# Optimization experiments

Hardware: AMD Instinct MI355X
Metric: run time of the kernel (lower is better)

The kernel has to match this reference:

```python
import jax, jax.numpy as jnp
import numpy as np

B, L, DIM = 1, 2048, 512
DHEAD = 64
HEADS = DIM // DHEAD  # 8
KS = 127              # kernel_size (odd)
EXP = 4


def setup_inputs() -> dict:
    key = jax.random.key(0)
    ks = jax.random.split(key, 8)
    sc = 0.02
    rnd = lambda k, shape: (jax.random.normal(k, shape, jnp.float32) * sc)
    return {
        "x": jax.random.normal(ks[0], (B, L, DIM), jnp.float32),
        "ln1_g": jnp.ones((DIM,), jnp.float32),
        "ln1_b": jnp.zeros((DIM,), jnp.float32),
        "qkv_w": rnd(ks[1], (DIM, 3 * DIM)),
        "qkv_b": jnp.zeros((3 * DIM,), jnp.float32),
        "rpb": rnd(ks[2], (HEADS, 2 * KS - 1)),
        "proj_w": rnd(ks[3], (DIM, DIM)),
        "proj_b": jnp.zeros((DIM,), jnp.float32),
        "ln2_g": jnp.ones((DIM,), jnp.float32),
        "ln2_b": jnp.zeros((DIM,), jnp.float32),
        "ff1_w": rnd(ks[4], (DIM, DIM * EXP)),
        "ff1_b": jnp.zeros((DIM * EXP,), jnp.float32),
        "ff2_w": rnd(ks[5], (DIM * EXP, DIM)),
        "ff2_b": jnp.zeros((DIM,), jnp.float32),
    }


def _layernorm(x, g, b, eps=1e-5):
    m = x.mean(-1, keepdims=True)
    v = ((x - m) ** 2).mean(-1, keepdims=True)
    return (x - m) * jax.lax.rsqrt(v + eps) * g + b


def _neighborhood_attn_1d(x, qkv_w, qkv_b, rpb, proj_w, proj_b):
    # NATTEN NeighborhoodAttention1D: window of KS keys per query, clamped
    # at sequence edges so every query sees exactly KS keys (requires L >= KS).
    b, l, dim = x.shape
    qkv = (x @ qkv_w + qkv_b).reshape(b, l, 3, HEADS, DHEAD)
    q, k, v = qkv[:, :, 0], qkv[:, :, 1], qkv[:, :, 2]  # [b,l,h,d]
    scale = DHEAD ** -0.5
    # window start per query, clamped to stay in-bounds
    starts = jnp.clip(jnp.arange(l) - KS // 2, 0, l - KS)          # [l]
    idx = starts[:, None] + jnp.arange(KS)                         # [l,KS]
    kg = k[:, idx]                                                 # [b,l,KS,h,d]
    vg = v[:, idx]                                                 # [b,l,KS,h,d]
    logits = jnp.einsum('blhd,blkhd->blhk', q * scale, kg)         # [b,l,h,KS]
    # relative-position bias: index = (j - i) + (KS - 1), in [0, 2KS-2]
    bias_idx = idx - jnp.arange(l)[:, None] + (KS - 1)             # [l,KS]
    logits = logits + rpb[:, bias_idx].transpose(1, 0, 2)[None]    # [1,l,h,KS]
    attn = jax.nn.softmax(logits, axis=-1)
    out = jnp.einsum('blhk,blkhd->blhd', attn, vg).reshape(b, l, dim)
    return out @ proj_w + proj_b


def reference(x, ln1_g, ln1_b, qkv_w, qkv_b, rpb, proj_w, proj_b,
              ln2_g, ln2_b, ff1_w, ff1_b, ff2_w, ff2_b):
    x = x + _neighborhood_attn_1d(_layernorm(x, ln1_g, ln1_b),
                                  qkv_w, qkv_b, rpb, proj_w, proj_b)
    h = _layernorm(x, ln2_g, ln2_b)
    h = jax.nn.gelu(h @ ff1_w + ff1_b, approximate=False) @ ff2_w + ff2_b
    return x + h
```

## Files before the change

kernel.cpp:

```cpp
#include <hip/hip_runtime.h>
#include <hip/hip_bf16.h>

static constexpr int Lc     = 2048;
static constexpr int DIMc   = 512;
static constexpr int HEADSc = 8;
static constexpr int DHEADc = 64;
static constexpr int KSc    = 127;
static constexpr int NQKVc  = 1536;

typedef __attribute__((ext_vector_type(8))) short short8;
typedef __attribute__((ext_vector_type(4))) float f32x4;
typedef unsigned short u16;
typedef unsigned int u32;

__device__ __forceinline__ float b2f(u16 s) {
  return __uint_as_float(((u32)s) << 16);
}
__device__ __forceinline__ u16 f2b(float x) {
  u32 u = __float_as_uint(x);
  return (u16)((u + 0x7fffu + ((u >> 16) & 1u)) >> 16);
}
__device__ __forceinline__ void gload16(const void* g, void* l) {
  __builtin_amdgcn_global_load_lds(
      (const __attribute__((address_space(1))) u32*)g,
      (__attribute__((address_space(3))) u32*)l, 16, 0, 0);
}

__global__ __launch_bounds__(256) void prep_kernel(
    const float* __restrict__ w0, const float* __restrict__ w1,
    const float* __restrict__ w2, const float* __restrict__ w3,
    u16* __restrict__ o0, u16* __restrict__ o1, u16* __restrict__ o2,
    u16* __restrict__ o3, const float* __restrict__ xin,
    const float* __restrict__ g, const float* __restrict__ b,
    u16* __restrict__ lnout) {
  __shared__ float tl[32][33];
  __shared__ float rs[4], rq[4], stat[2];
  const int tid = threadIdx.x;
  if (blockIdx.x >= 3072) {
    const int row = blockIdx.x - 3072;
    const float* rp = xin + (size_t)row * DIMc;
    float v0 = rp[tid];
    float v1 = rp[tid + 256];
    float s = v0 + v1;
    float sq = v0 * v0 + v1 * v1;
#pragma unroll
    for (int o = 32; o > 0; o >>= 1) {
      s += __shfl_down(s, o);
      sq += __shfl_down(sq, o);
    }
    const int wid = tid >> 6, lane = tid & 63;
    if (lane == 0) { rs[wid] = s; rq[wid] = sq; }
    __syncthreads();
    if (tid == 0) {
      float S = rs[0] + rs[1] + rs[2] + rs[3];
      float Q = rq[0] + rq[1] + rq[2] + rq[3];
      float m = S / DIMc;
      float var = Q / DIMc - m * m;
      stat[0] = m;
      stat[1] = rsqrtf(var + 1e-5f);
    }
    __syncthreads();
    const float m = stat[0], r = stat[1];
    lnout[(size_t)row * DIMc + tid] = f2b((v0 - m) * r * g[tid] + b[tid]);
    lnout[(size_t)row * DIMc + tid + 256] =
        f2b((v1 - m) * r * g[tid + 256] + b[tid + 256]);
    return;
  }
  int t = blockIdx.x;
  const float* W;
  u16* O;
  int K, N;
  if (t < 768)       { W = w0; O = o0; K = 512;  N = 1536; }
  else if (t < 1024) { W = w1; O = o1; K = 512;  N = 512;  t -= 768; }
  else if (t < 2048) { W = w2; O = o2; K = 512;  N = 2048; t -= 1024; }
  else               { W = w3; O = o3; K = 2048; N = 512;  t -= 2048; }
  const int nt = N >> 5;
  const int by = t / nt, bx = t % nt;
  const int c = tid & 31, r0 = tid >> 5;
#pragma unroll
  for (int i = 0; i < 4; ++i) {
    const int r = r0 + i * 8;
    tl[r][c] = W[(size_t)(by * 32 + r) * N + bx * 32 + c];
  }
  __syncthreads();
#pragma unroll
  for (int i = 0; i < 4; ++i) {
    const int r = r0 + i * 8;
    O[(size_t)(bx * 32 + r) * K + by * 32 + c] = f2b(tl[c][r]);
  }
}

__global__ __launch_bounds__(256) void ln2_kernel(const float* __restrict__ in,
                                                  const float* __restrict__ g,
                                                  const float* __restrict__ b,
                                                  u16* __restrict__ out) {
  const int row = blockIdx.x;
  const int tid = threadIdx.x;
  const float* rp = in + (size_t)row * DIMc;
  float v0 = rp[tid];
  float v1 = rp[tid + 256];
  float s = v0 + v1;
  float sq = v0 * v0 + v1 * v1;
  __shared__ float rs[4], rq[4], stat[2];
#pragma unroll
  for (int o = 32; o > 0; o >>= 1) {
    s += __shfl_down(s, o);
    sq += __shfl_down(sq, o);
  }
  const int wid = tid >> 6, lane = tid & 63;
  if (lane == 0) { rs[wid] = s; rq[wid] = sq; }
  __syncthreads();
  if (tid == 0) {
    float S = rs[0] + rs[1] + rs[2] + rs[3];
    float Q = rq[0] + rq[1] + rq[2] + rq[3];
    float m = S / DIMc;
    float var = Q / DIMc - m * m;
    stat[0] = m;
    stat[1] = rsqrtf(var + 1e-5f);
  }
  __syncthreads();
  const float m = stat[0], r = stat[1];
  out[(size_t)row * DIMc + tid] = f2b((v0 - m) * r * g[tid] + b[tid]);
  out[(size_t)row * DIMc + tid + 256] =
      f2b((v1 - m) * r * g[tid + 256] + b[tid + 256]);
}

template <int OP, typename OUT_T>
__global__ __launch_bounds__(128) void mfma_gemm(
    const u16* __restrict__ A, const u16* __restrict__ Bt,
    const float* __restrict__ bias, const float* __restrict__ res,
    OUT_T* __restrict__ C, int M, int N, int K) {
  constexpr int BK = 64;
  __shared__ __align__(16) u16 As[2][64 * BK];
  __shared__ __align__(16) u16 Bs[2][64 * BK];
  const int tid = threadIdx.x;
  const int wave = tid >> 6, lane = tid & 63;
  const int m0 = blockIdx.y * 64, n0 = blockIdx.x * 64;
  const int wn = wave * 32;
  const int T = K / BK;

  f32x4 acc[4][2] = {};

  const int fr = lane & 15;
  const int hi = lane >> 4;

  const int lrow = wave * 8 + (lane >> 3);
  const int lcol = ((lane & 7) ^ (lane >> 3)) * 8;

#define STAGE(k0, buf)                                                        \
  {                                                                           \
    _Pragma("unroll") for (int p = 0; p < 4; ++p) {                           \
      gload16(A + (size_t)(m0 + p * 16 + lrow) * K + (k0) + lcol,             \
              &As[buf][p * 1024 + wave * 512]);                               \
      gload16(Bt + (size_t)(n0 + p * 16 + lrow) * K + (k0) + lcol,            \
              &Bs[buf][p * 1024 + wave * 512]);                               \
    }                                                                         \
  }

  STAGE(0, 0);
  STAGE(BK, 1);

  for (int t = 0; t < T; ++t) {
    const int cur = t & 1;
    if (t + 1 < T) {
      asm volatile("s_waitcnt vmcnt(8)" ::: "memory");
    } else {
      asm volatile("s_waitcnt vmcnt(0)" ::: "memory");
    }
    __builtin_amdgcn_s_barrier();

    short8 af[4][2], bf[2][2];
#pragma unroll
    for (int i = 0; i < 4; ++i) {
      const int row = i * 16 + fr;
      const char* rb = (const char*)As[cur] + row * 128;
#pragma unroll
      for (int ks = 0; ks < 2; ++ks)
        af[i][ks] =
            *(const short8*)(rb + ((ks * 64 + hi * 16) ^ ((fr & 7) << 4)));
    }
#pragma unroll
    for (int j = 0; j < 2; ++j) {
      const int row = wn + j * 16 + fr;
      const char* rb = (const char*)Bs[cur] + row * 128;
#pragma unroll
      for (int ks = 0; ks < 2; ++ks)
        bf[j][ks] =
            *(const short8*)(rb + ((ks * 64 + hi * 16) ^ ((fr & 7) << 4)));
    }
    asm volatile("s_waitcnt lgkmcnt(0)" ::: "memory");
    __builtin_amdgcn_sched_barrier(0);
    __builtin_amdgcn_s_barrier();

    if (t + 2 < T) STAGE((t + 2) * BK, cur);

#pragma unroll
    for (int ks = 0; ks < 2; ++ks)
#pragma unroll
      for (int i = 0; i < 4; ++i)
#pragma unroll
        for (int j = 0; j < 2; ++j)
          acc[i][j] = __builtin_amdgcn_mfma_f32_16x16x32_bf16(
              af[i][ks], bf[j][ks], acc[i][j], 0, 0, 0);
  }
#undef STAGE

  const int cl = lane & 15;
  const int rbase = (lane >> 4) * 4;
#pragma unroll
  for (int i = 0; i < 4; ++i) {
#pragma unroll
    for (int j = 0; j < 2; ++j) {
      const int c = n0 + wn + j * 16 + cl;
      const float bv = bias[c];
#pragma unroll
      for (int r = 0; r < 4; ++r) {
        const int row = m0 + i * 16 + rbase + r;
        float v = acc[i][j][r] + bv;
        if (OP == 1) v = 0.5f * v * (1.0f + erff(v * 0.70710678118f));
        ((u16*)C)[(size_t)row * N + c] = f2b(v);
      }
    }
  }
}

__global__ __launch_bounds__(256, 1) void mfma_gemm_ks(
    const u16* __restrict__ A, const u16* __restrict__ Bt,
    const float* __restrict__ bias, const float* __restrict__ res,
    float* __restrict__ C, int M, int N, int K) {
  constexpr int BK = 32;
  __shared__ __align__(16) char LB[65536];
  const int tid = threadIdx.x;
  const int wave = tid >> 6, lane = tid & 63;
  const int m0 = blockIdx.y * 64, n0 = blockIdx.x * 64;
  const int kslice = K >> 2;
  const int kbeg = wave * kslice;
  const int T = kslice / BK;
  char* myb = LB + wave * 16384;

  f32x4 acc[4][4] = {};
  const int fr = lane & 15;
  const int hi = lane >> 4;

  const int lrow = lane >> 2;
  const int lcol = ((lane & 3) ^ ((lane >> 2) & 3)) * 8;

#define KSTAGE(k0, b)                                                         \
  {                                                                           \
    _Pragma("unroll") for (int p = 0; p < 4; ++p) {                           \
      gload16(A + (size_t)(m0 + p * 16 + lrow) * K + (k0) + lcol,             \
              myb + (b) * 8192 + p * 1024);                                   \
      gload16(Bt + (size_t)(n0 + p * 16 + lrow) * K + (k0) + lcol,            \
              myb + (b) * 8192 + 4096 + p * 1024);                            \
    }                                                                         \
  }

  KSTAGE(kbeg, 0);
  KSTAGE(kbeg + BK, 1);

  for (int t = 0; t < T; ++t) {
    const int cur = t & 1;
    if (t + 1 < T) {
      asm volatile("s_waitcnt vmcnt(8)" ::: "memory");
    } else {
      asm volatile("s_waitcnt vmcnt(0)" ::: "memory");
    }

    short8 af[4], bf[4];
#pragma unroll
    for (int i = 0; i < 4; ++i) {
      const char* rb = myb + cur * 8192 + (i * 16 + fr) * 64;
      af[i] = *(const short8*)(rb + ((hi * 16) ^ ((fr & 3) << 4)));
    }
#pragma unroll
    for (int j = 0; j < 4; ++j) {
      const char* rb = myb + cur * 8192 + 4096 + (j * 16 + fr) * 64;
      bf[j] = *(const short8*)(rb + ((hi * 16) ^ ((fr & 3) << 4)));
    }
    asm volatile("s_waitcnt lgkmcnt(0)" ::: "memory");
    __builtin_amdgcn_sched_barrier(0);

    if (t + 2 < T) KSTAGE(kbeg + (t + 2) * BK, cur);

    __builtin_amdgcn_s_setprio(1);
#pragma unroll
    for (int i = 0; i < 4; ++i)
#pragma unroll
      for (int j = 0; j < 4; ++j)
        acc[i][j] = __builtin_amdgcn_mfma_f32_16x16x32_bf16(af[i], bf[j],
                                                            acc[i][j], 0, 0, 0);
    __builtin_amdgcn_s_setprio(0);
  }
#undef KSTAGE

  __syncthreads();
  float* red = (float*)LB;
  const int rbase = hi * 4;
#pragma unroll
  for (int i = 0; i < 4; ++i)
#pragma unroll
    for (int j = 0; j < 4; ++j)
#pragma unroll
      for (int r = 0; r < 4; ++r)
        red[wave * 4096 + (i * 16 + rbase + r) * 64 + j * 16 + fr] =
            acc[i][j][r];
  __syncthreads();
#pragma unroll
  for (int q = 0; q < 4; ++q) {
    const int idx = q * 1024 + tid * 4;
    const int row = idx >> 6, col = idx & 63;
    f32x4 s = *(const f32x4*)&red[idx];
#pragma unroll
    for (int w = 1; w < 4; ++w) s += *(const f32x4*)&red[w * 4096 + idx];
    const f32x4 bb = *(const f32x4*)&bias[n0 + col];
    const size_t o = (size_t)(m0 + row) * N + n0 + col;
    const f32x4 rr = *(const f32x4*)&res[o];
    s += bb + rr;
    *(f32x4*)&C[o] = s;
  }
}

__global__ __launch_bounds__(256) void attn_mfma(const u16* __restrict__ qkv,
                                                 const float* __restrict__ rpb,
                                                 u16* __restrict__ out) {
  constexpr int NR = 192, NT = 12, PP = 200;
  __shared__ __align__(16) u16 Ks[NR * DHEADc];
  __shared__ __align__(16) u16 Vt[DHEADc * NR];
  __shared__ __align__(16) u16 Ps[4][16 * PP];
  __shared__ float rp[2 * KSc - 1];
  const int h = blockIdx.y, l0 = blockIdx.x * 64, tid = threadIdx.x;
  const int wv = tid >> 6, lane = tid & 63;
  const int fr = lane & 15, hi = lane >> 4;

  int s_min = l0 - 63;
  if (s_min < 0) s_min = 0;
  if (s_min > Lc - KSc) s_min = Lc - KSc;

  for (int i = tid; i < 2 * KSc - 1; i += 256) rp[i] = rpb[h * (2 * KSc - 1) + i];

#pragma unroll
  for (int rd = 0; rd < 6; ++rd) {
    const int linear = rd * 4096 + wv * 1024 + lane * 16;
    const int row = linear >> 7;
    const int seg = (linear >> 4) & 7;
    const int segp = seg ^ (row & 7);
    int gl = s_min + row;
    if (gl > Lc - 1) gl = Lc - 1;
    gload16(qkv + (size_t)gl * NQKVc + DIMc + h * DHEADc + segp * 8,
            (char*)Ks + rd * 4096 + wv * 1024);
  }

#pragma unroll
  for (int rd = 0; rd < 3; ++rd) {
    const int t = rd * 256 + tid;
    const int rpair = t >> 3, seg = t & 7;
    const int r0 = rpair * 2;
    int g0 = s_min + r0, g1 = s_min + r0 + 1;
    if (g0 > Lc - 1) g0 = Lc - 1;
    if (g1 > Lc - 1) g1 = Lc - 1;
    const short8 a =
        *(const short8*)(qkv + (size_t)g0 * NQKVc + 2 * DIMc + h * DHEADc + seg * 8);
    const short8 bq =
        *(const short8*)(qkv + (size_t)g1 * NQKVc + 2 * DIMc + h * DHEADc + seg * 8);
#pragma unroll
    for (int j = 0; j < 8; ++j) {
      const int d = seg * 8 + j;
      int byte = d * (NR * 2) + r0 * 2;
      byte ^= (d & 7) << 4;
      *(u32*)((char*)Vt + byte) =
          ((u32)(u16)a[j]) | (((u32)(u16)bq[j]) << 16);
    }
  }

  const int lq = l0 + wv * 16 + fr;
  short8 qf[2];
#pragma unroll
  for (int ks = 0; ks < 2; ++ks)
    qf[ks] = *(const short8*)(qkv + (size_t)lq * NQKVc + h * DHEADc + ks * 32 + hi * 8);

  __syncthreads();

  f32x4 S[NT] = {};
  __builtin_amdgcn_s_setprio(1);
#pragma unroll
  for (int jt = 0; jt < NT; ++jt) {
#pragma unroll
    for (int ks = 0; ks < 2; ++ks) {
      int byte = (jt * 16 + fr) * 128 + ks * 64 + hi * 16;
      byte ^= (fr & 7) << 4;
      const short8 kf = *(const short8*)((const char*)Ks + byte);
      S[jt] = __builtin_amdgcn_mfma_f32_16x16x32_bf16(qf[ks], kf, S[jt], 0, 0, 0);
    }
  }
  __builtin_amdgcn_s_setprio(0);

  float inv4[4];
#pragma unroll
  for (int r = 0; r < 4; ++r) {
    const int l = l0 + wv * 16 + hi * 4 + r;
    int st = l - 63;
    if (st < 0) st = 0;
    if (st > Lc - KSc) st = Lc - KSc;
    float mx = -3e38f;
#pragma unroll
    for (int jt = 0; jt < NT; ++jt) {
      const int pos = s_min + jt * 16 + fr;
      const int j = pos - st;
      float v = -3e38f;
      if (j >= 0 && j <= KSc - 1) v = S[jt][r] * 0.125f + rp[pos - l + KSc - 1];
      S[jt][r] = v;
      mx = fmaxf(mx, v);
    }
#pragma unroll
    for (int o = 1; o < 16; o <<= 1) mx = fmaxf(mx, __shfl_xor(mx, o));
    float sum = 0.f;
#pragma unroll
    for (int jt = 0; jt < NT; ++jt) {
      const float e = __expf(S[jt][r] - mx);
      S[jt][r] = e;
      sum += e;
    }
#pragma unroll
    for (int o = 1; o < 16; o <<= 1) sum += __shfl_xor(sum, o);
    inv4[r] = 1.f / sum;
  }

#pragma unroll
  for (int jt = 0; jt < NT; ++jt)
#pragma unroll
    for (int r = 0; r < 4; ++r)
      Ps[wv][(hi * 4 + r) * PP + jt * 16 + fr] = f2b(S[jt][r] * inv4[r]);

  f32x4 O[4] = {};
  __builtin_amdgcn_s_setprio(1);
#pragma unroll
  for (int ks = 0; ks < 6; ++ks) {
    const short8 pa =
        *(const short8*)((const char*)Ps[wv] + fr * (PP * 2) + ks * 64 + hi * 16);
#pragma unroll
    for (int dt = 0; dt < 4; ++dt) {
      int byte = (dt * 16 + fr) * (NR * 2) + ks * 64 + hi * 16;
      byte ^= (fr & 7) << 4;
      const short8 vb = *(const short8*)((const char*)Vt + byte);
      O[dt] = __builtin_amdgcn_mfma_f32_16x16x32_bf16(pa, vb, O[dt], 0, 0, 0);
    }
  }
  __builtin_amdgcn_s_setprio(0);

#pragma unroll
  for (int dt = 0; dt < 4; ++dt)
#pragma unroll
    for (int r = 0; r < 4; ++r)
      out[(size_t)(l0 + wv * 16 + hi * 4 + r) * DIMc + h * DHEADc + dt * 16 + fr] =
          f2b(O[dt][r]);
}

extern "C" void kernel_launch(void* const* d_in, const int* in_sizes, int n_in,
                              void* d_out, int out_size, void* d_ws,
                              size_t ws_size, hipStream_t stream) {
  const float* x      = (const float*)d_in[0];
  const float* ln1_g  = (const float*)d_in[1];
  const float* ln1_b  = (const float*)d_in[2];
  const float* qkv_w  = (const float*)d_in[3];
  const float* qkv_b  = (const float*)d_in[4];
  const float* rpb    = (const float*)d_in[5];
  const float* proj_w = (const float*)d_in[6];
  const float* proj_b = (const float*)d_in[7];
  const float* ln2_g  = (const float*)d_in[8];
  const float* ln2_b  = (const float*)d_in[9];
  const float* ff1_w  = (const float*)d_in[10];
  const float* ff1_b  = (const float*)d_in[11];
  const float* ff2_w  = (const float*)d_in[12];
  const float* ff2_b  = (const float*)d_in[13];
  float* out = (float*)d_out;

  char* ws = (char*)d_ws;
  u16*   lnbuf   = (u16*)(ws);
  u16*   qkvbuf  = (u16*)(ws + ((size_t)2  << 20));
  u16*   attnbuf = (u16*)(ws + ((size_t)8  << 20));
  float* x2      = (float*)(ws + ((size_t)10 << 20));
  u16*   ff1buf  = (u16*)(ws + ((size_t)14 << 20));
  u16*   wt_qkv  = (u16*)(ws + ((size_t)22 << 20));
  u16*   wt_proj = (u16*)(ws + ((size_t)23 << 20) + ((size_t)512 << 10));
  u16*   wt_ff1  = (u16*)(ws + ((size_t)24 << 20));
  u16*   wt_ff2  = (u16*)(ws + ((size_t)26 << 20));

  prep_kernel<<<5120, 256, 0, stream>>>(qkv_w, proj_w, ff1_w, ff2_w, wt_qkv,
                                        wt_proj, wt_ff1, wt_ff2, x, ln1_g,
                                        ln1_b, lnbuf);
  mfma_gemm<0, u16><<<dim3(NQKVc / 64, Lc / 64), 128, 0, stream>>>(
      lnbuf, wt_qkv, qkv_b, nullptr, qkvbuf, Lc, NQKVc, DIMc);
  attn_mfma<<<dim3(Lc / 64, HEADSc), 256, 0, stream>>>(qkvbuf, rpb, attnbuf);
  mfma_gemm_ks<<<dim3(DIMc / 64, Lc / 64), 256, 0, stream>>>(
      attnbuf, wt_proj, proj_b, x, x2, Lc, DIMc, DIMc);
  ln2_kernel<<<Lc, 256, 0, stream>>>(x2, ln2_g, ln2_b, lnbuf);
  mfma_gemm<1, u16><<<dim3(4 * DIMc / 64, Lc / 64), 128, 0, stream>>>(
      lnbuf, wt_ff1, ff1_b, nullptr, ff1buf, Lc, 4 * DIMc, DIMc);
  mfma_gemm_ks<<<dim3(DIMc / 64, Lc / 64), 256, 0, stream>>>(
      ff1buf, wt_ff2, ff2_b, x2, out, Lc, DIMc, 4 * DIMc);
}
```

Baseline: 67.05 us.

## Fold non-QKV weight transposes into the QKV GEMM launch and vectorize transposes

The prep kernel now transposes and converts only the QKV weight and runs LayerNorm1. The proj, ff1 and ff2 weight transposes move into extra blocks of a new fused QKV GEMM kernel, so that memory-bound conversion work runs alongside the compute-bound GEMM tiles instead of delaying it. The transpose tiles also switch to float4 loads and packed ushort4 stores. In exchange, the GEMM kernel carries extra LDS for the transpose tile and a branch, which may reduce occupancy for the GEMM blocks.

```diff
diff --git a/kernel.cpp b/kernel.cpp
--- a/kernel.cpp
+++ b/kernel.cpp
@@ -27,17 +27,14 @@
 }
 
 __global__ __launch_bounds__(256) void prep_kernel(
-    const float* __restrict__ w0, const float* __restrict__ w1,
-    const float* __restrict__ w2, const float* __restrict__ w3,
-    u16* __restrict__ o0, u16* __restrict__ o1, u16* __restrict__ o2,
-    u16* __restrict__ o3, const float* __restrict__ xin,
-    const float* __restrict__ g, const float* __restrict__ b,
-    u16* __restrict__ lnout) {
+    const float* __restrict__ w0, u16* __restrict__ o0,
+    const float* __restrict__ xin, const float* __restrict__ g,
+    const float* __restrict__ b, u16* __restrict__ lnout) {
   __shared__ float tl[32][33];
   __shared__ float rs[4], rq[4], stat[2];
   const int tid = threadIdx.x;
-  if (blockIdx.x >= 3072) {
-    const int row = blockIdx.x - 3072;
+  if (blockIdx.x >= 768) {
+    const int row = blockIdx.x - 768;
     const float* rp = xin + (size_t)row * DIMc;
     float v0 = rp[tid];
     float v1 = rp[tid + 256];
@@ -66,27 +63,23 @@
         f2b((v1 - m) * r * g[tid + 256] + b[tid + 256]);
     return;
   }
-  int t = blockIdx.x;
-  const float* W;
-  u16* O;
-  int K, N;
-  if (t < 768)       { W = w0; O = o0; K = 512;  N = 1536; }
-  else if (t < 1024) { W = w1; O = o1; K = 512;  N = 512;  t -= 768; }
-  else if (t < 2048) { W = w2; O = o2; K = 512;  N = 2048; t -= 1024; }
-  else               { W = w3; O = o3; K = 2048; N = 512;  t -= 2048; }
-  const int nt = N >> 5;
-  const int by = t / nt, bx = t % nt;
-  const int c = tid & 31, r0 = tid >> 5;
-#pragma unroll
-  for (int i = 0; i < 4; ++i) {
-    const int r = r0 + i * 8;
-    tl[r][c] = W[(size_t)(by * 32 + r) * N + bx * 32 + c];
+  const int t = blockIdx.x;
+  const int nt = NQKVc >> 5;
+  const int byw = t / nt, bxw = t % nt;
+  const int c4 = tid & 7, r = tid >> 3;
+  {
+    const f32x4 v =
+        *(const f32x4*)(w0 + (size_t)(byw * 32 + r) * NQKVc + bxw * 32 + c4 * 4);
+    tl[r][c4 * 4 + 0] = v[0];
+    tl[r][c4 * 4 + 1] = v[1];
+    tl[r][c4 * 4 + 2] = v[2];
+    tl[r][c4 * 4 + 3] = v[3];
   }
   __syncthreads();
-#pragma unroll
-  for (int i = 0; i < 4; ++i) {
-    const int r = r0 + i * 8;
-    O[(size_t)(bx * 32 + r) * K + by * 32 + c] = f2b(tl[c][r]);
+  {
+    ushort4 pk = {f2b(tl[c4 * 4 + 0][r]), f2b(tl[c4 * 4 + 1][r]),
+                  f2b(tl[c4 * 4 + 2][r]), f2b(tl[c4 * 4 + 3][r])};
+    *(ushort4*)(o0 + (size_t)(bxw * 32 + r) * DIMc + byw * 32 + c4 * 4) = pk;
   }
 }
 
@@ -123,6 +116,139 @@
   out[(size_t)row * DIMc + tid] = f2b((v0 - m) * r * g[tid] + b[tid]);
   out[(size_t)row * DIMc + tid + 256] =
       f2b((v1 - m) * r * g[tid + 256] + b[tid + 256]);
+}
+
+__global__ __launch_bounds__(128) void qkv_wtrans_kernel(
+    const u16* __restrict__ A, const u16* __restrict__ Bt,
+    const float* __restrict__ bias, u16* __restrict__ C,
+    const float* __restrict__ w1, const float* __restrict__ w2,
+    const float* __restrict__ w3, u16* __restrict__ o1, u16* __restrict__ o2,
+    u16* __restrict__ o3) {
+  constexpr int BK = 64, K = DIMc, N = NQKVc;
+  __shared__ __align__(16) u16 As[2][64 * BK];
+  __shared__ __align__(16) u16 Bs[2][64 * BK];
+  __shared__ float tl[32][33];
+  const int tid = threadIdx.x;
+
+  if (blockIdx.x >= 768) {
+    int t = blockIdx.x - 768;
+    const float* W;
+    u16* O;
+    int WK, WN;
+    if (t < 256)       { W = w1; O = o1; WK = 512;  WN = 512;  }
+    else if (t < 1280) { W = w2; O = o2; WK = 512;  WN = 2048; t -= 256; }
+    else               { W = w3; O = o3; WK = 2048; WN = 512;  t -= 1280; }
+    const int nt = WN >> 5;
+    const int byw = t / nt, bxw = t % nt;
+    const int c4 = tid & 7, r0 = tid >> 3;
+#pragma unroll
+    for (int i = 0; i < 2; ++i) {
+      const int r = r0 + i * 16;
+      const f32x4 v =
+          *(const f32x4*)(W + (size_t)(byw * 32 + r) * WN + bxw * 32 + c4 * 4);
+      tl[r][c4 * 4 + 0] = v[0];
+      tl[r][c4 * 4 + 1] = v[1];
+      tl[r][c4 * 4 + 2] = v[2];
+      tl[r][c4 * 4 + 3] = v[3];
+    }
+    __syncthreads();
+#pragma unroll
+    for (int i = 0; i < 2; ++i) {
+      const int r = r0 + i * 16;
+      ushort4 pk = {f2b(tl[c4 * 4 + 0][r]), f2b(tl[c4 * 4 + 1][r]),
+                    f2b(tl[c4 * 4 + 2][r]), f2b(tl[c4 * 4 + 3][r])};
+      *(ushort4*)(O + (size_t)(bxw * 32 + r) * WK + byw * 32 + c4 * 4) = pk;
+    }
+    return;
+  }
+
+  const int b = blockIdx.x;
+  const int wave = tid >> 6, lane = tid & 63;
+  const int m0 = (b / 24) * 64, n0 = (b % 24) * 64;
+  const int wn = wave * 32;
+  const int T = K / BK;
+
+  f32x4 acc[4][2] = {};
+
+  const int fr = lane & 15;
+  const int hi = lane >> 4;
+
+  const int lrow = wave * 8 + (lane >> 3);
+  const int lcol = ((lane & 7) ^ (lane >> 3)) * 8;
+
+#define STAGE(k0, buf)                                                        \
+  {                                                                           \
+    _Pragma("unroll") for (int p = 0; p < 4; ++p) {                           \
+      gload16(A + (size_t)(m0 + p * 16 + lrow) * K + (k0) + lcol,             \
+              &As[buf][p * 1024 + wave * 512]);                               \
+      gload16(Bt + (size_t)(n0 + p * 16 + lrow) * K + (k0) + lcol,            \
+              &Bs[buf][p * 1024 + wave * 512]);                               \
+    }                                                                         \
+  }
+
+  STAGE(0, 0);
+  STAGE(BK, 1);
+
+  for (int t = 0; t < T; ++t) {
+    const int cur = t & 1;
+    if (t + 1 < T) {
+      asm volatile("s_waitcnt vmcnt(8)" ::: "memory");
+    } else {
+      asm volatile("s_waitcnt vmcnt(0)" ::: "memory");
+    }
+    __builtin_amdgcn_s_barrier();
+
+    short8 af[4][2], bf[2][2];
+#pragma unroll
+    for (int i = 0; i < 4; ++i) {
+      const int row = i * 16 + fr;
+      const char* rb = (const char*)As[cur] + row * 128;
+#pragma unroll
+      for (int ks = 0; ks < 2; ++ks)
+        af[i][ks] =
+            *(const short8*)(rb + ((ks * 64 + hi * 16) ^ ((fr & 7) << 4)));
+    }
+#pragma unroll
+    for (int j = 0; j < 2; ++j) {
+      const int row = wn + j * 16 + fr;
+      const char* rb = (const char*)Bs[cur] + row * 128;
+#pragma unroll
+      for (int ks = 0; ks < 2; ++ks)
+        bf[j][ks] =
+            *(const short8*)(rb + ((ks * 64 + hi * 16) ^ ((fr & 7) << 4)));
+    }
+    asm volatile("s_waitcnt lgkmcnt(0)" ::: "memory");
+    __builtin_amdgcn_sched_barrier(0);
+    __builtin_amdgcn_s_barrier();
+
+    if (t + 2 < T) STAGE((t + 2) * BK, cur);
+
+#pragma unroll
+    for (int ks = 0; ks < 2; ++ks)
+#pragma unroll
+      for (int i = 0; i < 4; ++i)
+#pragma unroll
+        for (int j = 0; j < 2; ++j)
+          acc[i][j] = __builtin_amdgcn_mfma_f32_16x16x32_bf16(
+              af[i][ks], bf[j][ks], acc[i][j], 0, 0, 0);
+  }
+#undef STAGE
+
+  const int cl = lane & 15;
+  const int rbase = (lane >> 4) * 4;
+#pragma unroll
+  for (int i = 0; i < 4; ++i) {
+#pragma unroll
+    for (int j = 0; j < 2; ++j) {
+      const int c = n0 + wn + j * 16 + cl;
+      const float bv = bias[c];
+#pragma unroll
+      for (int r = 0; r < 4; ++r) {
+        const int row = m0 + i * 16 + rbase + r;
+        C[(size_t)row * N + c] = f2b(acc[i][j][r] + bv);
+      }
+    }
+  }
 }
 
 template <int OP, typename OUT_T>
@@ -485,11 +611,10 @@
   u16*   wt_ff1  = (u16*)(ws + ((size_t)24 << 20));
   u16*   wt_ff2  = (u16*)(ws + ((size_t)26 << 20));
 
-  prep_kernel<<<5120, 256, 0, stream>>>(qkv_w, proj_w, ff1_w, ff2_w, wt_qkv,
-                                        wt_proj, wt_ff1, wt_ff2, x, ln1_g,
-                                        ln1_b, lnbuf);
-  mfma_gemm<0, u16><<<dim3(NQKVc / 64, Lc / 64), 128, 0, stream>>>(
-      lnbuf, wt_qkv, qkv_b, nullptr, qkvbuf, Lc, NQKVc, DIMc);
+  prep_kernel<<<2816, 256, 0, stream>>>(qkv_w, wt_qkv, x, ln1_g, ln1_b, lnbuf);
+  qkv_wtrans_kernel<<<3072, 128, 0, stream>>>(lnbuf, wt_qkv, qkv_b, qkvbuf,
+                                              proj_w, ff1_w, ff2_w, wt_proj,
+                                              wt_ff1, wt_ff2);
   attn_mfma<<<dim3(Lc / 64, HEADSc), 256, 0, stream>>>(qkvbuf, rpb, attnbuf);
   mfma_gemm_ks<<<dim3(DIMc / 64, Lc / 64), 256, 0, stream>>>(
       attnbuf, wt_proj, proj_b, x, x2, Lc, DIMc, DIMc);
```

After: 68.20 us. No clear change (+1.7%).
